# Kernel tuning notes

Measured on AMD Instinct MI355X. Metric: run time of the kernel, lower is better.

The kernel has to match this reference:

```python
import jax, jax.numpy as jnp
import numpy as np

N, IN_F, OUT_F = 2048, 512, 512

def setup_inputs() -> dict:
    key = jax.random.key(0)
    kx, ka, kb = jax.random.split(key, 3)
    x = jax.random.uniform(kx, (N, IN_F), dtype=jnp.float32)          # inputs in [0,1]
    a = jax.random.uniform(ka, (OUT_F, IN_F), dtype=jnp.float32)      # weight in [0,1]
    b = jax.random.uniform(kb, (OUT_F,), dtype=jnp.float32)           # bias in [0,1]
    return {"x": x, "a": a, "b": b}

def reference(x, a, b):
    # Lukasiewicz / max-plus 'matmul':
    # y[n,o] = max(0, max_i(x[n,i] + a[o,i] - 1)), then max with bias b[o].
    inter = x[:, None, :] + a[None, :, :] - 1.0        # [N, out, in]
    y = jnp.maximum(jnp.max(inter, axis=-1), 0.0)      # [N, out]
    y = jnp.maximum(y, b[None, :])
    return y
```

## Files before the change

### kernel.cpp

```cpp
#include <hip/hip_runtime.h>
#include <cstdint>


#define TILE 64
#define BK   64
#define NROW 2048
#define NK   512
#define NCOL 512
#define KSPLIT 2
#define NKT  (NK / BK / KSPLIT)

typedef float f32x4 __attribute__((ext_vector_type(4)));

__device__ __forceinline__ void async_load16(const float* g, float* l) {
  __builtin_amdgcn_global_load_lds(
      (const __attribute__((address_space(1))) void*)g,
      (__attribute__((address_space(3))) void*)l,
      16, 0, 0);
}

__global__ __launch_bounds__(256) void luka_kernel(
    const float* __restrict__ X, const float* __restrict__ A,
    const float* __restrict__ Bv, float* __restrict__ Y) {
  __shared__ float xs[2][TILE * BK];
  __shared__ float as[2][TILE * BK];
  const int tid  = threadIdx.x;
  const int wave = tid >> 6;
  const int tx   = tid & 15;
  const int ty   = tid >> 4;
  const int rowBase = blockIdx.y * TILE;
  const int colBase = blockIdx.x * TILE;
  const int ktBase  = blockIdx.z * NKT;

  uint32_t xoff[4], aoff[4];
#pragma unroll
  for (int r = 0; r < 4; ++r) {
    int row = ty * 4 + r;
    xoff[r] = (uint32_t)row * 256u + ((uint32_t)((row & 15) ^ (row >> 2)) << 4);
  }
#pragma unroll
  for (int c = 0; c < 4; ++c) {
    int row = tx * 4 + c;
    aoff[c] = (uint32_t)row * 256u + ((uint32_t)((row & 15) ^ (row >> 2)) << 4);
  }

  float acc[4][4];
#pragma unroll
  for (int r = 0; r < 4; ++r)
#pragma unroll
    for (int c = 0; c < 4; ++c) acc[r][c] = 0.0f;

  const int row0 = tid >> 4;
  const int sl   = tid & 15;

  auto stage = [&](int buf, int kt) {
#pragma unroll
    for (int j = 0; j < 4; ++j) {
      int row = row0 + j * 16;
      int m   = (row & 15) ^ (row >> 2);
      int kk  = ((sl ^ m) << 2);
      const float* gx = X + (size_t)(rowBase + row) * NK + kt * BK + kk;
      const float* ga = A + (size_t)(colBase + row) * NK + kt * BK + kk;
      async_load16(gx, &xs[buf][j * 1024 + wave * 256]);
      async_load16(ga, &as[buf][j * 1024 + wave * 256]);
    }
  };

  stage(0, ktBase);
  __syncthreads();

  int buf = 0;
#pragma unroll 1
  for (int t = 0; t < NKT; ++t) {
    if (t < NKT - 1) stage(buf ^ 1, ktBase + t + 1);

    const char* xb = (const char*)&xs[buf][0];
    const char* ab = (const char*)&as[buf][0];
#pragma unroll
    for (int s4 = 0; s4 < BK / 4; ++s4) {
      f32x4 xf[4], af[4];
#pragma unroll
      for (int r = 0; r < 4; ++r)
        xf[r] = *(const f32x4*)(xb + (xoff[r] ^ (uint32_t)(s4 << 4)));
#pragma unroll
      for (int c = 0; c < 4; ++c)
        af[c] = *(const f32x4*)(ab + (aoff[c] ^ (uint32_t)(s4 << 4)));
#pragma unroll
      for (int r = 0; r < 4; ++r) {
#pragma unroll
        for (int c = 0; c < 4; ++c) {
          f32x4 s = xf[r] + af[c];
          float t0 = fmaxf(fmaxf(s.x, s.y), acc[r][c]);
          acc[r][c] = fmaxf(fmaxf(s.z, s.w), t0);
        }
      }
    }
    __syncthreads();
    buf ^= 1;
  }

  const f32x4 bv = *(const f32x4*)&Bv[colBase + tx * 4];
  float bvv[4] = {bv.x, bv.y, bv.z, bv.w};
  int* Yi = (int*)Y;
#pragma unroll
  for (int r = 0; r < 4; ++r) {
    int base = (rowBase + ty * 4 + r) * NCOL + colBase + tx * 4;
#pragma unroll
    for (int c = 0; c < 4; ++c) {
      float t = fmaxf(fmaxf(acc[r][c] - 1.0f, bvv[c]), 0.0f);
      atomicMax(&Yi[base + c], __float_as_int(t));
    }
  }
}

extern "C" void kernel_launch(void* const* d_in, const int* in_sizes, int n_in,
                              void* d_out, int out_size, void* d_ws, size_t ws_size,
                              hipStream_t stream) {
  const float* X = (const float*)d_in[0];
  const float* A = (const float*)d_in[1];
  const float* B = (const float*)d_in[2];
  float* Y = (float*)d_out;
  hipMemsetAsync(Y, 0, (size_t)out_size * sizeof(float), stream);
  dim3 grid(NCOL / TILE, NROW / TILE, KSPLIT);
  luka_kernel<<<grid, dim3(256), 0, stream>>>(X, A, B, Y);
}
```

Measured before the change: 98.91 us.

## Pretranspose weights and compute register-resident columns with broadcast X rows

Adds a prep kernel that repacks A into a k-major float4 layout in workspace. A new main kernel has each thread own one output column and 8 rows, streaming A from global memory with prefetch and reading X rows uniformly across the wave, with no LDS. The fallback LDS kernel drops the K-split, so the memset and atomicMax are replaced with plain vector stores. This trades LDS tiling reuse for simpler global and broadcast loads, at the cost of an extra prep launch.

```diff
diff --git a/kernel.cpp b/kernel.cpp
--- a/kernel.cpp
+++ b/kernel.cpp
@@ -2,36 +2,78 @@
 #include <cstdint>
 
 
-#define TILE 64
-#define BK   64
 #define NROW 2048
 #define NK   512
 #define NCOL 512
-#define KSPLIT 2
-#define NKT  (NK / BK / KSPLIT)
-
+#define RP   8
 typedef float f32x4 __attribute__((ext_vector_type(4)));
 
+__global__ __launch_bounds__(256) void luka_prep(const float* __restrict__ A,
+                                                 f32x4* __restrict__ Ap4) {
+  int idx = blockIdx.x * 256 + threadIdx.x;
+  int o  = idx >> 7;
+  int k4 = idx & 127;
+  f32x4 v = *(const f32x4*)(A + o * NK + k4 * 4);
+  Ap4[k4 * NCOL + o] = v;
+}
+
+__global__ __launch_bounds__(256) void luka_main(
+    const f32x4* __restrict__ Ap4, const float* __restrict__ X,
+    const float* __restrict__ Bv, float* __restrict__ Y) {
+  const int col  = blockIdx.y * 256 + threadIdx.x;
+  const int row0 = blockIdx.x * RP;
+
+  float acc[RP];
+#pragma unroll
+  for (int r = 0; r < RP; ++r) acc[r] = 0.0f;
+
+  f32x4 a[4], an[4];
+#pragma unroll
+  for (int j = 0; j < 4; ++j) a[j] = Ap4[j * NCOL + col];
+
+#pragma unroll 2
+  for (int k4 = 0; k4 < NK / 4; k4 += 4) {
+    if (k4 + 4 < NK / 4) {
+#pragma unroll
+      for (int j = 0; j < 4; ++j) an[j] = Ap4[(k4 + 4 + j) * NCOL + col];
+    }
+#pragma unroll
+    for (int r = 0; r < RP; ++r) {
+      const float* xp = X + (size_t)(row0 + r) * NK + k4 * 4;
+#pragma unroll
+      for (int j = 0; j < 4; ++j) {
+        f32x4 xv = *(const f32x4*)(xp + 4 * j);
+        f32x4 s  = a[j] + xv;
+        float t  = fmaxf(fmaxf(s.z, s.w), acc[r]);
+        acc[r]   = fmaxf(fmaxf(s.x, s.y), t);
+      }
+    }
+#pragma unroll
+    for (int j = 0; j < 4; ++j) a[j] = an[j];
+  }
+
+  const float bv = Bv[col];
+#pragma unroll
+  for (int r = 0; r < RP; ++r) {
+    float t = acc[r] - 1.0f;
+    Y[(size_t)(row0 + r) * NCOL + col] = fmaxf(fmaxf(t, bv), 0.0f);
+  }
+}
+
+#define TILE 64
+#define BK   64
 __device__ __forceinline__ void async_load16(const float* g, float* l) {
   __builtin_amdgcn_global_load_lds(
       (const __attribute__((address_space(1))) void*)g,
-      (__attribute__((address_space(3))) void*)l,
-      16, 0, 0);
+      (__attribute__((address_space(3))) void*)l, 16, 0, 0);
 }
-
-__global__ __launch_bounds__(256) void luka_kernel(
+__global__ __launch_bounds__(256) void luka_fb(
     const float* __restrict__ X, const float* __restrict__ A,
     const float* __restrict__ Bv, float* __restrict__ Y) {
   __shared__ float xs[2][TILE * BK];
   __shared__ float as[2][TILE * BK];
-  const int tid  = threadIdx.x;
-  const int wave = tid >> 6;
-  const int tx   = tid & 15;
-  const int ty   = tid >> 4;
-  const int rowBase = blockIdx.y * TILE;
-  const int colBase = blockIdx.x * TILE;
-  const int ktBase  = blockIdx.z * NKT;
-
+  const int tid = threadIdx.x, wave = tid >> 6, tx = tid & 15, ty = tid >> 4;
+  const int rowBase = blockIdx.y * TILE, colBase = blockIdx.x * TILE;
   uint32_t xoff[4], aoff[4];
 #pragma unroll
   for (int r = 0; r < 4; ++r) {
@@ -43,37 +85,30 @@
     int row = tx * 4 + c;
     aoff[c] = (uint32_t)row * 256u + ((uint32_t)((row & 15) ^ (row >> 2)) << 4);
   }
-
   float acc[4][4];
 #pragma unroll
   for (int r = 0; r < 4; ++r)
 #pragma unroll
     for (int c = 0; c < 4; ++c) acc[r][c] = 0.0f;
-
-  const int row0 = tid >> 4;
-  const int sl   = tid & 15;
-
+  const int row0 = tid >> 4, sl = tid & 15;
   auto stage = [&](int buf, int kt) {
 #pragma unroll
     for (int j = 0; j < 4; ++j) {
       int row = row0 + j * 16;
-      int m   = (row & 15) ^ (row >> 2);
-      int kk  = ((sl ^ m) << 2);
-      const float* gx = X + (size_t)(rowBase + row) * NK + kt * BK + kk;
-      const float* ga = A + (size_t)(colBase + row) * NK + kt * BK + kk;
-      async_load16(gx, &xs[buf][j * 1024 + wave * 256]);
-      async_load16(ga, &as[buf][j * 1024 + wave * 256]);
+      int m = (row & 15) ^ (row >> 2);
+      int kk = ((sl ^ m) << 2);
+      async_load16(X + (size_t)(rowBase + row) * NK + kt * BK + kk,
+                   &xs[buf][j * 1024 + wave * 256]);
+      async_load16(A + (size_t)(colBase + row) * NK + kt * BK + kk,
+                   &as[buf][j * 1024 + wave * 256]);
     }
   };
-
-  stage(0, ktBase);
+  stage(0, 0);
   __syncthreads();
-
   int buf = 0;
 #pragma unroll 1
-  for (int t = 0; t < NKT; ++t) {
-    if (t < NKT - 1) stage(buf ^ 1, ktBase + t + 1);
-
+  for (int kt = 0; kt < NK / BK; ++kt) {
+    if (kt < NK / BK - 1) stage(buf ^ 1, kt + 1);
     const char* xb = (const char*)&xs[buf][0];
     const char* ab = (const char*)&as[buf][0];
 #pragma unroll
@@ -86,30 +121,27 @@
       for (int c = 0; c < 4; ++c)
         af[c] = *(const f32x4*)(ab + (aoff[c] ^ (uint32_t)(s4 << 4)));
 #pragma unroll
-      for (int r = 0; r < 4; ++r) {
+      for (int r = 0; r < 4; ++r)
 #pragma unroll
         for (int c = 0; c < 4; ++c) {
           f32x4 s = xf[r] + af[c];
           float t0 = fmaxf(fmaxf(s.x, s.y), acc[r][c]);
           acc[r][c] = fmaxf(fmaxf(s.z, s.w), t0);
         }
-      }
     }
     __syncthreads();
     buf ^= 1;
   }
-
   const f32x4 bv = *(const f32x4*)&Bv[colBase + tx * 4];
   float bvv[4] = {bv.x, bv.y, bv.z, bv.w};
-  int* Yi = (int*)Y;
 #pragma unroll
   for (int r = 0; r < 4; ++r) {
-    int base = (rowBase + ty * 4 + r) * NCOL + colBase + tx * 4;
-#pragma unroll
-    for (int c = 0; c < 4; ++c) {
-      float t = fmaxf(fmaxf(acc[r][c] - 1.0f, bvv[c]), 0.0f);
-      atomicMax(&Yi[base + c], __float_as_int(t));
-    }
+    f32x4 o;
+    o.x = fmaxf(fmaxf(acc[r][0] - 1.0f, bvv[0]), 0.0f);
+    o.y = fmaxf(fmaxf(acc[r][1] - 1.0f, bvv[1]), 0.0f);
+    o.z = fmaxf(fmaxf(acc[r][2] - 1.0f, bvv[2]), 0.0f);
+    o.w = fmaxf(fmaxf(acc[r][3] - 1.0f, bvv[3]), 0.0f);
+    *(f32x4*)&Y[(size_t)(rowBase + ty * 4 + r) * NCOL + colBase + tx * 4] = o;
   }
 }
 
@@ -120,7 +152,14 @@
   const float* A = (const float*)d_in[1];
   const float* B = (const float*)d_in[2];
   float* Y = (float*)d_out;
-  hipMemsetAsync(Y, 0, (size_t)out_size * sizeof(float), stream);
-  dim3 grid(NCOL / TILE, NROW / TILE, KSPLIT);
-  luka_kernel<<<grid, dim3(256), 0, stream>>>(X, A, B, Y);
+
+  if (ws_size >= (size_t)NCOL * NK * sizeof(float)) {
+    f32x4* Ap4 = (f32x4*)d_ws;
+    luka_prep<<<dim3(NCOL * NK / 4 / 256), dim3(256), 0, stream>>>(A, Ap4);
+    dim3 grid(NROW / RP, NCOL / 256);
+    luka_main<<<grid, dim3(256), 0, stream>>>(Ap4, X, B, Y);
+  } else {
+    dim3 grid(NCOL / TILE, NROW / TILE);
+    luka_fb<<<grid, dim3(256), 0, stream>>>(X, A, B, Y);
+  }
 }
```

Result: slower. 123.8 us (+25.1%).
